# Kernel tuning notes

Measured on AMD Instinct MI355X. Metric: run time of the kernel, lower is better.

## Reference

```python
import jax, jax.numpy as jnp
import numpy as np

BLOCKS, LAYERS, KS = 4, 2, 2
DILATIONS = [2 ** i for _ in range(BLOCKS) for i in range(LAYERS)]  # [1,2]*4
B, C_IN, N, T = 16, 2, 2048, 12
RC, DC, SC, EC, OUT = 32, 32, 256, 512, 12
L = BLOCKS * LAYERS
BN_EPS = 1e-5


def setup_inputs() -> dict:
    key = jax.random.key(0)
    ks = jax.random.split(key, 24)
    # raw inputs
    x = jax.random.normal(ks[0], (B, C_IN, N, T), dtype=jnp.float32)
    # two fixed supports: row-normalized random adjacency (dense, as in GraphWaveNet transition matrices)
    A_raw = jax.random.uniform(ks[1], (2, N, N), dtype=jnp.float32)
    A = A_raw / jnp.sum(A_raw, axis=2, keepdims=True)
    nodevec1 = jax.random.normal(ks[2], (N, 10), dtype=jnp.float32)
    nodevec2 = jax.random.normal(ks[3], (10, N), dtype=jnp.float32)
    s = 0.1  # weight scale to keep activations in a sane range
    filter_w = jax.random.normal(ks[4], (L, DC, RC, KS), dtype=jnp.float32) * s
    filter_b = jax.random.normal(ks[5], (L, DC), dtype=jnp.float32) * s
    gate_w = jax.random.normal(ks[6], (L, DC, RC, KS), dtype=jnp.float32) * s
    gate_b = jax.random.normal(ks[7], (L, DC), dtype=jnp.float32) * s
    skip_w = jax.random.normal(ks[8], (L, SC, DC), dtype=jnp.float32) * s
    skip_b = jax.random.normal(ks[9], (L, SC), dtype=jnp.float32) * s
    gcn_w = jax.random.normal(ks[10], (L, RC, 7 * DC), dtype=jnp.float32) * s
    gcn_b = jax.random.normal(ks[11], (L, RC), dtype=jnp.float32) * s
    bn_gamma = 1.0 + 0.1 * jax.random.normal(ks[12], (L, RC), dtype=jnp.float32)
    bn_beta = 0.1 * jax.random.normal(ks[13], (L, RC), dtype=jnp.float32)
    bn_mean = 0.1 * jax.random.normal(ks[14], (L, RC), dtype=jnp.float32)
    bn_var = 1.0 + jax.random.uniform(ks[15], (L, RC), dtype=jnp.float32)
    start_w = jax.random.normal(ks[16], (RC, C_IN), dtype=jnp.float32) * s
    start_b = jax.random.normal(ks[17], (RC,), dtype=jnp.float32) * s
    end1_w = jax.random.normal(ks[18], (EC, SC), dtype=jnp.float32) * s
    end1_b = jax.random.normal(ks[19], (EC,), dtype=jnp.float32) * s
    end2_w = jax.random.normal(ks[20], (OUT, EC), dtype=jnp.float32) * s
    end2_b = jax.random.normal(ks[21], (OUT,), dtype=jnp.float32) * s
    return dict(x=x, A=A, nodevec1=nodevec1, nodevec2=nodevec2,
                filter_w=filter_w, filter_b=filter_b, gate_w=gate_w, gate_b=gate_b,
                skip_w=skip_w, skip_b=skip_b, gcn_w=gcn_w, gcn_b=gcn_b,
                bn_gamma=bn_gamma, bn_beta=bn_beta, bn_mean=bn_mean, bn_var=bn_var,
                start_w=start_w, start_b=start_b, end1_w=end1_w, end1_b=end1_b,
                end2_w=end2_w, end2_b=end2_b)


def _conv1x1(x, w, b):
    # x: [b,c,n,t], w: [o,c] -> [b,o,n,t]
    return jnp.einsum('oc,bcnt->bont', w, x) + b[None, :, None, None]


def _dilated_conv2(x, w, b, d):
    # kernel (1,2) with time dilation d; out length T-d (valid conv)
    xa, xb = x[..., :-d], x[..., d:]
    y = jnp.einsum('oc,bcnt->bont', w[:, :, 0], xa) + jnp.einsum('oc,bcnt->bont', w[:, :, 1], xb)
    return y + b[None, :, None, None]


def _fwd(x, A, nodevec1, nodevec2, filter_w, filter_b, gate_w, gate_b,
         skip_w, skip_b, gcn_w, gcn_b, bn_gamma, bn_beta, bn_mean, bn_var,
         start_w, start_b, end1_w, end1_b, end2_w, end2_b):
    # pad 1 step at the start of time; T becomes 13 == receptive_field
    x = jnp.pad(x, ((0, 0), (0, 0), (0, 0), (1, 0)))
    x = x[:, :2]
    x = _conv1x1(x, start_w, start_b)  # [B,RC,N,13]
    # adaptive adjacency
    adp = jax.nn.softmax(jax.nn.relu(nodevec1 @ nodevec2), axis=1)
    supports = [A[0], A[1], adp]
    skip = None
    for i, d in enumerate(DILATIONS):
        residual = x
        filt = jnp.tanh(_dilated_conv2(residual, filter_w[i], filter_b[i], d))
        gate = jax.nn.sigmoid(_dilated_conv2(residual, gate_w[i], gate_b[i], d))
        x = filt * gate  # [B,DC,N,T-d]
        s = _conv1x1(x, skip_w[i], skip_b[i])  # [B,SC,N,T']
        skip = s if skip is None else s + skip[..., -s.shape[3]:]
        # GCN: order-2 diffusion over 3 supports, concat, 1x1 mix (dropout is identity in eval)
        outs = [x]
        for a in supports:
            x1 = jnp.einsum('bcvt,vw->bcwt', x, a)
            x2 = jnp.einsum('bcvt,vw->bcwt', x1, a)
            outs.extend([x1, x2])
        h = jnp.concatenate(outs, axis=1)  # [B,7*DC,N,T']
        x = _conv1x1(h, gcn_w[i], gcn_b[i])
        x = x + residual[..., -x.shape[3]:]
        # BatchNorm2d in eval mode (running stats)
        inv = bn_gamma[i] / jnp.sqrt(bn_var[i] + BN_EPS)
        x = (x - bn_mean[i][None, :, None, None]) * inv[None, :, None, None] + bn_beta[i][None, :, None, None]
    x = jax.nn.relu(skip)
    x = jax.nn.relu(_conv1x1(x, end1_w, end1_b))
    x = _conv1x1(x, end2_w, end2_b)  # [B,OUT,N,1]
    return x


def reference(x, A, nodevec1, nodevec2, filter_w, filter_b, gate_w, gate_b,
              skip_w, skip_b, gcn_w, gcn_b, bn_gamma, bn_beta, bn_mean, bn_var,
              start_w, start_b, end1_w, end1_b, end2_w, end2_b):
    return _fwd(x, A, nodevec1, nodevec2, filter_w, filter_b, gate_w, gate_b,
                skip_w, skip_b, gcn_w, gcn_b, bn_gamma, bn_beta, bn_mean, bn_var,
                start_w, start_b, end1_w, end1_b, end2_w, end2_b)
```

## Files before the change

### kernel.cpp

```cpp
#include <hip/hip_runtime.h>
#include <math.h>


#define NNODE 2048
#define NLAYER 8
#define SSTR ((size_t)NNODE * NNODE)

typedef unsigned short u16;
typedef unsigned int u32;
typedef __attribute__((ext_vector_type(8))) short bf16x8;
typedef __attribute__((ext_vector_type(4))) float f32x4;

__device__ __forceinline__ u16 f2bf(float f) {
    unsigned u = __builtin_bit_cast(unsigned, f);
    u += 0x7fffu + ((u >> 16) & 1u);
    return (u16)(u >> 16);
}
__device__ __forceinline__ float bf2f(u16 h) {
    unsigned u = ((unsigned)h) << 16;
    return __builtin_bit_cast(float, u);
}
__device__ __forceinline__ float bflo(u32 p) { return __builtin_bit_cast(float, p << 16); }
__device__ __forceinline__ float bfhi(u32 p) { return __builtin_bit_cast(float, p & 0xffff0000u); }
__device__ __forceinline__ u32 pack2(float a, float b) {
    return (u32)f2bf(a) | ((u32)f2bf(b) << 16);
}

__device__ __forceinline__ void gld16(const void* g, void* l) {
    __builtin_amdgcn_global_load_lds(
        (const __attribute__((address_space(1))) unsigned int*)g,
        (__attribute__((address_space(3))) unsigned int*)l, 16, 0, 0);
}

__global__ __launch_bounds__(256) void k_adp_mm(const float* __restrict__ nv1,
                                                const float* __restrict__ nv2,
                                                float* __restrict__ P) {
    int v = blockIdx.y;
    int w = blockIdx.x * 256 + threadIdx.x;
    float acc = 0.f;
#pragma unroll
    for (int k = 0; k < 10; ++k) acc += nv1[v * 10 + k] * nv2[k * NNODE + w];
    P[(size_t)v * NNODE + w] = acc;
}

__global__ __launch_bounds__(256) void k_softmax(float* __restrict__ P) {
    int v = blockIdx.x, tid = threadIdx.x;
    float* row = P + (size_t)v * NNODE;
    float m = 0.f;
    for (int w = tid; w < NNODE; w += 256) m = fmaxf(m, fmaxf(row[w], 0.f));
#pragma unroll
    for (int off = 32; off > 0; off >>= 1) m = fmaxf(m, __shfl_down(m, off));
    __shared__ float redm[4];
    __shared__ float reds[4];
    int wave = tid >> 6, lane = tid & 63;
    if (lane == 0) redm[wave] = m;
    __syncthreads();
    m = fmaxf(fmaxf(redm[0], redm[1]), fmaxf(redm[2], redm[3]));
    float s = 0.f;
    for (int w = tid; w < NNODE; w += 256) s += expf(fmaxf(row[w], 0.f) - m);
#pragma unroll
    for (int off = 32; off > 0; off >>= 1) s += __shfl_down(s, off);
    if (lane == 0) reds[wave] = s;
    __syncthreads();
    s = reds[0] + reds[1] + reds[2] + reds[3];
    float inv = 1.f / s;
    for (int w = tid; w < NNODE; w += 256) row[w] = expf(fmaxf(row[w], 0.f) - m) * inv;
}

__global__ __launch_bounds__(256) void k_transp(const float* __restrict__ A,
                                                const float* __restrict__ adp,
                                                u16* __restrict__ ST,
                                                u16* __restrict__ Sbf) {
    __shared__ float tile[32][33];
    int s = blockIdx.z;
    const float* src = (s < 2) ? (A + (size_t)s * SSTR) : adp;
    int v0 = blockIdx.y * 32, w0 = blockIdx.x * 32;
    int tx = threadIdx.x & 31, ty = threadIdx.x >> 5;
    u16* dst2 = Sbf + (size_t)s * SSTR;
#pragma unroll
    for (int p = 0; p < 4; ++p) {
        float v = src[(size_t)(v0 + ty + p * 8) * NNODE + w0 + tx];
        tile[ty + p * 8][tx] = v;
        dst2[(size_t)(v0 + ty + p * 8) * NNODE + w0 + tx] = f2bf(v);
    }
    __syncthreads();
    u16* dst = ST + (size_t)(2 * s) * SSTR;
#pragma unroll
    for (int p = 0; p < 4; ++p)
        dst[(size_t)(w0 + ty + p * 8) * NNODE + v0 + tx] = f2bf(tile[tx][ty + p * 8]);
}

__global__ __launch_bounds__(256) void k_gemm_mfma(
    const u16* __restrict__ A, int lda, size_t asstr,
    const u16* __restrict__ BT, size_t bsstr,
    u16* __restrict__ C, int ldc, size_t csstr, int sbase) {
    __shared__ u16 Asl[128 * 32];
    __shared__ u16 Bsl[128 * 32];
    const int tid = threadIdx.x;
    const int wave = tid >> 6, lane = tid & 63;
    const int sidx = sbase + blockIdx.z;
    const u16* Ab = A + sidx * asstr + (size_t)blockIdx.y * 128 * lda;
    const u16* Bb = BT + sidx * bsstr + (size_t)blockIdx.x * 128 * NNODE;
    const int tr = tid >> 2;
    const int tc = (tid & 3) * 8;
    char* AslB = (char*)Asl + wave * 1024;
    char* BslB = (char*)Bsl + wave * 1024;
    const int wm = (wave & 1) * 64, wn = (wave >> 1) * 64;
    const int fr = lane & 15;
    const int fk = (lane >> 4) * 8;
    f32x4 acc[4][4];
#pragma unroll
    for (int i = 0; i < 4; ++i)
#pragma unroll
        for (int j = 0; j < 4; ++j) acc[i][j] = (f32x4){0.f, 0.f, 0.f, 0.f};

    for (int k0 = 0; k0 < 2048; k0 += 32) {
        gld16(Ab + (size_t)tr * lda + k0 + tc, AslB);
        gld16(Ab + (size_t)(tr + 64) * lda + k0 + tc, AslB + 4096);
        gld16(Bb + (size_t)tr * NNODE + k0 + tc, BslB);
        gld16(Bb + (size_t)(tr + 64) * NNODE + k0 + tc, BslB + 4096);
        __syncthreads();
        bf16x8 af[4], bf[4];
#pragma unroll
        for (int i = 0; i < 4; ++i)
            af[i] = *(const bf16x8*)&Asl[(wm + i * 16 + fr) * 32 + fk];
#pragma unroll
        for (int j = 0; j < 4; ++j)
            bf[j] = *(const bf16x8*)&Bsl[(wn + j * 16 + fr) * 32 + fk];
#pragma unroll
        for (int i = 0; i < 4; ++i)
#pragma unroll
            for (int j = 0; j < 4; ++j)
                acc[i][j] = __builtin_amdgcn_mfma_f32_16x16x32_bf16(af[i], bf[j], acc[i][j], 0, 0, 0);
        __syncthreads();
    }
    u16* Cb = C + sidx * csstr + (size_t)(blockIdx.y * 128 + wm) * ldc + blockIdx.x * 128 + wn;
    const int orow = (lane >> 4) * 4;
#pragma unroll
    for (int i = 0; i < 4; ++i)
#pragma unroll
        for (int j = 0; j < 4; ++j)
#pragma unroll
            for (int r = 0; r < 4; ++r)
                Cb[(size_t)(i * 16 + orow + r) * ldc + j * 16 + fr] = f2bf(acc[i][j][r]);
}

__global__ __launch_bounds__(512, 2) void k_gemmZ(const u16* __restrict__ Xg,
                                                  const u16* __restrict__ ST,
                                                  u16* __restrict__ Z, int pass) {
    __shared__ __align__(16) char ldsb[131072];
    const int tid = threadIdx.x;
    const int wave = tid >> 6, lane = tid & 63;
    const int m0 = blockIdx.y * 256;
    const int slice = pass * 3 + (blockIdx.x >> 3);
    const int n0 = (blockIdx.x & 7) * 256;
    const u16* AbG = Xg + (size_t)m0 * 2048;
    const u16* BbG = ST + (size_t)slice * SSTR + (size_t)n0 * 2048;

    const int xorc = ((tid & 7) ^ ((tid >> 3) & 7)) << 3;
    const size_t aRow = (size_t)(tid >> 3) * 2048 + xorc;
    const int bRowLoc = ((tid >> 8) << 6) + (((tid >> 6) & 3) << 3) + ((tid >> 3) & 7);
    const size_t bRow = (size_t)bRowLoc * 2048 + xorc;
    const int aw = wave << 10;
    const int bw = ((wave >> 2) << 13) + ((wave & 3) << 10);

    const int fr = lane & 15;
    const int cl4 = lane >> 4;
    const int ch0 = (cl4 ^ (fr & 7)) << 4;
    const int ch1 = ch0 ^ 64;
    const int aRd = ((wave & 1) << 14) + fr * 128;
    const int bRd = ((wave >> 1) << 13) + fr * 128;
    const int wm = (wave & 1) << 7;
    const int wn = (wave >> 1) << 6;

    char* A0 = ldsb;
    char* A1 = ldsb + 32768;
    char* B0 = ldsb + 65536;
    char* B1 = ldsb + 98304;

    auto STA = [&](char* Abase, int k0, int q) {
        const size_t g = (size_t)(q << 6) * 2048 + aRow + k0;
        gld16(AbG + g, Abase + (q << 13) + aw);
        gld16(AbG + g + (size_t)128 * 2048, Abase + 16384 + (q << 13) + aw);
    };
    auto STB = [&](char* Bbase, int k0, int q) {
        const size_t g = (size_t)(q << 5) * 2048 + bRow + k0;
        gld16(BbG + g, Bbase + (q << 12) + bw);
        gld16(BbG + g + (size_t)128 * 2048, Bbase + 16384 + (q << 12) + bw);
    };

    f32x4 acc[8][4];
#pragma unroll
    for (int i = 0; i < 8; ++i)
#pragma unroll
        for (int j = 0; j < 4; ++j) acc[i][j] = (f32x4){0.f, 0.f, 0.f, 0.f};

    STA(A0, 0, 0); STA(A0, 0, 1); STB(B0, 0, 0); STB(B0, 0, 1);
    STA(A1, 64, 0); STB(B1, 64, 0); STB(B1, 64, 1);
    asm volatile("s_waitcnt vmcnt(6)" ::: "memory");
    asm volatile("s_barrier" ::: "memory");

    char *Ac = A0, *Ao = A1, *Bc = B0, *Bo = B1;
    bf16x8 af[4][2], bfl[2][2], bfh[2][2];

    for (int T = 0; T < 32; ++T) {
#pragma unroll
        for (int i = 0; i < 4; ++i) {
            af[i][0] = *(const bf16x8*)(Ac + aRd + (i << 11) + ch0);
            af[i][1] = *(const bf16x8*)(Ac + aRd + (i << 11) + ch1);
        }
#pragma unroll
        for (int j = 0; j < 2; ++j) {
            bfl[j][0] = *(const bf16x8*)(Bc + bRd + (j << 11) + ch0);
            bfl[j][1] = *(const bf16x8*)(Bc + bRd + (j << 11) + ch1);
        }
        if (T < 31) STA(Ao, (T + 1) * 64, 1);
        asm volatile("s_barrier" ::: "memory");
        asm volatile("s_waitcnt lgkmcnt(0)" ::: "memory");
        __builtin_amdgcn_sched_barrier(0);
        __builtin_amdgcn_s_setprio(1);
#pragma unroll
        for (int i = 0; i < 4; ++i)
#pragma unroll
            for (int j = 0; j < 2; ++j) {
                acc[i][j] = __builtin_amdgcn_mfma_f32_16x16x32_bf16(af[i][0], bfl[j][0], acc[i][j], 0, 0, 0);
                acc[i][j] = __builtin_amdgcn_mfma_f32_16x16x32_bf16(af[i][1], bfl[j][1], acc[i][j], 0, 0, 0);
            }
        __builtin_amdgcn_s_setprio(0);
        asm volatile("s_barrier" ::: "memory");
#pragma unroll
        for (int j = 0; j < 2; ++j) {
            bfh[j][0] = *(const bf16x8*)(Bc + bRd + 4096 + (j << 11) + ch0);
            bfh[j][1] = *(const bf16x8*)(Bc + bRd + 4096 + (j << 11) + ch1);
        }
        if (T < 30) STA(Ac, (T + 2) * 64, 0);
        asm volatile("s_barrier" ::: "memory");
        asm volatile("s_waitcnt lgkmcnt(0)" ::: "memory");
        __builtin_amdgcn_sched_barrier(0);
        __builtin_amdgcn_s_setprio(1);
#pragma unroll
        for (int i = 0; i < 4; ++i)
#pragma unroll
            for (int j = 0; j < 2; ++j) {
                acc[i][2 + j] = __builtin_amdgcn_mfma_f32_16x16x32_bf16(af[i][0], bfh[j][0], acc[i][2 + j], 0, 0, 0);
                acc[i][2 + j] = __builtin_amdgcn_mfma_f32_16x16x32_bf16(af[i][1], bfh[j][1], acc[i][2 + j], 0, 0, 0);
            }
        __builtin_amdgcn_s_setprio(0);
        asm volatile("s_barrier" ::: "memory");
#pragma unroll
        for (int i = 0; i < 4; ++i) {
            af[i][0] = *(const bf16x8*)(Ac + aRd + 8192 + (i << 11) + ch0);
            af[i][1] = *(const bf16x8*)(Ac + aRd + 8192 + (i << 11) + ch1);
        }
        if (T < 30) STB(Bc, (T + 2) * 64, 0);
        asm volatile("s_barrier" ::: "memory");
        asm volatile("s_waitcnt lgkmcnt(0)" ::: "memory");
        __builtin_amdgcn_sched_barrier(0);
        __builtin_amdgcn_s_setprio(1);
#pragma unroll
        for (int i = 0; i < 4; ++i)
#pragma unroll
            for (int j = 0; j < 2; ++j) {
                acc[4 + i][2 + j] = __builtin_amdgcn_mfma_f32_16x16x32_bf16(af[i][0], bfh[j][0], acc[4 + i][2 + j], 0, 0, 0);
                acc[4 + i][2 + j] = __builtin_amdgcn_mfma_f32_16x16x32_bf16(af[i][1], bfh[j][1], acc[4 + i][2 + j], 0, 0, 0);
            }
        __builtin_amdgcn_s_setprio(0);
        asm volatile("s_barrier" ::: "memory");
        if (T < 30) STB(Bc, (T + 2) * 64, 1);
        asm volatile("s_barrier" ::: "memory");
        __builtin_amdgcn_sched_barrier(0);
        __builtin_amdgcn_s_setprio(1);
#pragma unroll
        for (int i = 0; i < 4; ++i)
#pragma unroll
            for (int j = 0; j < 2; ++j) {
                acc[4 + i][j] = __builtin_amdgcn_mfma_f32_16x16x32_bf16(af[i][0], bfl[j][0], acc[4 + i][j], 0, 0, 0);
                acc[4 + i][j] = __builtin_amdgcn_mfma_f32_16x16x32_bf16(af[i][1], bfl[j][1], acc[4 + i][j], 0, 0, 0);
            }
        __builtin_amdgcn_s_setprio(0);
        if (T < 30) {
            asm volatile("s_waitcnt vmcnt(6)" ::: "memory");
        } else if (T == 30) {
            asm volatile("s_waitcnt vmcnt(0)" ::: "memory");
        }
        asm volatile("s_barrier" ::: "memory");
        char* t;
        t = Ac; Ac = Ao; Ao = t;
        t = Bc; Bc = Bo; Bo = t;
    }

    const int col0 = (blockIdx.x >> 3) * 2048 + (blockIdx.x & 7) * 256;
    u16* Cb = Z + (size_t)(m0 + wm) * 6144 + col0 + wn;
    const int orow = cl4 * 4;
#pragma unroll
    for (int i = 0; i < 8; ++i)
#pragma unroll
        for (int j = 0; j < 4; ++j)
#pragma unroll
            for (int r = 0; r < 4; ++r)
                Cb[(size_t)(i * 16 + orow + r) * 6144 + j * 16 + fr] = f2bf(acc[i][j][r]);
}

__global__ __launch_bounds__(256) void k_start(const float* __restrict__ xin,
                                               const float* __restrict__ sw,
                                               const float* __restrict__ sb,
                                               u16* __restrict__ out, int b0) {
    int n = blockIdx.x * 256 + threadIdx.x;
    int t = blockIdx.y;
    int bl = blockIdx.z;
    int b = b0 + bl;
    float x0 = 0.f, x1 = 0.f;
    if (t > 0) {
        x0 = xin[((size_t)(b * 2 + 0) * NNODE + n) * 12 + (t - 1)];
        x1 = xin[((size_t)(b * 2 + 1) * NNODE + n) * 12 + (t - 1)];
    }
#pragma unroll
    for (int co = 0; co < 32; ++co) {
        float v = sw[co * 2 + 0] * x0 + sw[co * 2 + 1] * x1 + sb[co];
        out[((size_t)(bl * 32 + co) * 13 + t) * NNODE + n] = f2bf(v);
    }
}

__global__ __launch_bounds__(256) void k_gate(const u16* __restrict__ cur,
                                              u16* __restrict__ xg,
                                              u16* __restrict__ nxt,
                                              int T, int Tn, int d,
                                              const float* __restrict__ fw,
                                              const float* __restrict__ fb,
                                              const float* __restrict__ gw,
                                              const float* __restrict__ gb,
                                              const float* __restrict__ gcwl,
                                              const float* __restrict__ gcbl,
                                              int donxt) {
    __shared__ float4 wp[1024];
    __shared__ float w0[32][33];
    int tid = threadIdx.x;
#pragma unroll
    for (int u = 0; u < 4; ++u) {
        int idx = tid + u * 256;
        int ci = idx >> 5, co = idx & 31;
        wp[idx] = make_float4(fw[co * 64 + ci * 2], fw[co * 64 + ci * 2 + 1],
                              gw[co * 64 + ci * 2], gw[co * 64 + ci * 2 + 1]);
        w0[ci][co] = gcwl[co * 224 + ci];
    }
    __syncthreads();
    int n = blockIdx.x * 512 + tid * 2;
    int t = blockIdx.y;
    int bl = blockIdx.z;
    float f0[32], f1[32], g0[32], g1[32];
#pragma unroll
    for (int co = 0; co < 32; ++co) { f0[co] = 0.f; f1[co] = 0.f; g0[co] = 0.f; g1[co] = 0.f; }
    for (int ci = 0; ci < 32; ++ci) {
        size_t ba = ((size_t)(bl * 32 + ci) * T + t) * NNODE + n;
        size_t bb = ((size_t)(bl * 32 + ci) * T + t + d) * NNODE + n;
        u32 ua = *(const u32*)&cur[ba];
        u32 ub = *(const u32*)&cur[bb];
        float xa0 = bflo(ua), xa1 = bfhi(ua);
        float xb0 = bflo(ub), xb1 = bfhi(ub);
#pragma unroll
        for (int co = 0; co < 32; ++co) {
            float4 w = wp[ci * 32 + co];
            f0[co] += w.x * xa0 + w.y * xb0;
            f1[co] += w.x * xa1 + w.y * xb1;
            g0[co] += w.z * xa0 + w.w * xb0;
            g1[co] += w.z * xa1 + w.w * xb1;
        }
    }
#pragma unroll
    for (int co = 0; co < 32; ++co) {
        float fbv = fb[co], gbv = gb[co];
        float a0 = tanhf(f0[co] + fbv) * (1.f / (1.f + expf(-(g0[co] + gbv))));
        float a1 = tanhf(f1[co] + fbv) * (1.f / (1.f + expf(-(g1[co] + gbv))));
        f0[co] = a0; f1[co] = a1;
        size_t o = ((size_t)(bl * 32 + co) * Tn + t) * NNODE + n;
        *(u32*)&xg[o] = pack2(a0, a1);
    }
    if (donxt) {
#pragma unroll
        for (int cop = 0; cop < 32; ++cop) {
            float s0 = gcbl[cop], s1 = s0;
#pragma unroll
            for (int ci = 0; ci < 32; ++ci) {
                float wv = w0[ci][cop];
                s0 += wv * f0[ci];
                s1 += wv * f1[ci];
            }
            size_t o = ((size_t)(bl * 32 + cop) * Tn + t) * NNODE + n;
            *(u32*)&nxt[o] = pack2(s0, s1);
        }
    }
}

__global__ __launch_bounds__(256) void k_skip(const u16* __restrict__ xg,
                                              float* __restrict__ skip, int Tn,
                                              const float* __restrict__ sw,
                                              const float* __restrict__ sb, int b0, int init) {
    __shared__ float wl[256];
    int tid = threadIdx.x;
    int sc0 = blockIdx.y * 8;
    wl[tid] = sw[sc0 * 32 + tid];
    __syncthreads();
    int n = blockIdx.x * 512 + tid * 2;
    int bl = blockIdx.z;
    float a0[8], a1[8];
#pragma unroll
    for (int j = 0; j < 8; ++j) { a0[j] = 0.f; a1[j] = 0.f; }
    for (int ci = 0; ci < 32; ci += 2) {
        u32 p0 = *(const u32*)&xg[((size_t)(bl * 32 + ci + 0) * Tn + (Tn - 1)) * NNODE + n];
        u32 p1 = *(const u32*)&xg[((size_t)(bl * 32 + ci + 1) * Tn + (Tn - 1)) * NNODE + n];
        float v00 = bflo(p0), v01 = bfhi(p0);
        float v10 = bflo(p1), v11 = bfhi(p1);
#pragma unroll
        for (int j = 0; j < 8; ++j) {
            float wA = wl[j * 32 + ci], wB = wl[j * 32 + ci + 1];
            a0[j] += wA * v00 + wB * v10;
            a1[j] += wA * v01 + wB * v11;
        }
    }
    int b = b0 + bl;
#pragma unroll
    for (int j = 0; j < 8; ++j) {
        size_t o = ((size_t)(b * 256) + sc0 + j) * NNODE + n;
        float bsv = sb[sc0 + j];
        if (init) {
            *(float2*)&skip[o] = make_float2(a0[j] + bsv, a1[j] + bsv);
        } else {
            float2 old = *(const float2*)&skip[o];
            *(float2*)&skip[o] = make_float2(old.x + a0[j] + bsv, old.y + a1[j] + bsv);
        }
    }
}

__global__ __launch_bounds__(256) void k_accum(const u16* __restrict__ Z,
                                               int cbase,
                                               const float* __restrict__ gcnw,
                                               u16* __restrict__ outp,
                                               const u16* __restrict__ resid,
                                               int Tn, int d, int finalf,
                                               const float* __restrict__ bng,
                                               const float* __restrict__ bnb,
                                               const float* __restrict__ bnm,
                                               const float* __restrict__ bnv) {
    __shared__ float wl[3][32][32];
    int tid = threadIdx.x;
    for (int u = tid; u < 3072; u += 256) {
        int g = u >> 10, ci = (u >> 5) & 31, co = u & 31;
        wl[g][ci][co] = gcnw[co * 224 + cbase + g * 32 + ci];
    }
    __syncthreads();
    int n = blockIdx.x * 512 + tid * 2;
    int t = blockIdx.y, bl = blockIdx.z;
    float a0[32], a1[32];
#pragma unroll
    for (int co = 0; co < 32; ++co) { a0[co] = 0.f; a1[co] = 0.f; }
    for (int ci = 0; ci < 32; ++ci) {
        size_t m = (size_t)(bl * 32 + ci) * Tn + t;
#pragma unroll
        for (int g = 0; g < 3; ++g) {
            u32 zz = *(const u32*)&Z[m * 6144 + g * 2048 + n];
            float v0 = bflo(zz), v1 = bfhi(zz);
#pragma unroll
            for (int cq = 0; cq < 8; ++cq) {
                float4 w = *(const float4*)&wl[g][ci][cq * 4];
                a0[cq * 4 + 0] += w.x * v0; a1[cq * 4 + 0] += w.x * v1;
                a0[cq * 4 + 1] += w.y * v0; a1[cq * 4 + 1] += w.y * v1;
                a0[cq * 4 + 2] += w.z * v0; a1[cq * 4 + 2] += w.z * v1;
                a0[cq * 4 + 3] += w.w * v0; a1[cq * 4 + 3] += w.w * v1;
            }
        }
    }
#pragma unroll
    for (int co = 0; co < 32; ++co) {
        size_t o = ((size_t)(bl * 32 + co) * Tn + t) * NNODE + n;
        u32 oo = *(const u32*)&outp[o];
        float v0 = bflo(oo) + a0[co];
        float v1 = bfhi(oo) + a1[co];
        if (finalf) {
            size_t ro = ((size_t)(bl * 32 + co) * (Tn + d) + t + d) * NNODE + n;
            u32 rr = *(const u32*)&resid[ro];
            v0 += bflo(rr); v1 += bfhi(rr);
            float inv = bng[co] * rsqrtf(bnv[co] + 1e-5f);
            float mu = bnm[co], be = bnb[co];
            v0 = (v0 - mu) * inv + be;
            v1 = (v1 - mu) * inv + be;
        }
        *(u32*)&outp[o] = pack2(v0, v1);
    }
}

__global__ __launch_bounds__(256) void k_skipT(const float* __restrict__ skip,
                                               u16* __restrict__ skipT) {
    __shared__ float tile[32][33];
    int b = blockIdx.z;
    int n0 = blockIdx.x * 32, c0 = blockIdx.y * 32;
    int tx = threadIdx.x & 31, ty = threadIdx.x >> 5;
#pragma unroll
    for (int p = 0; p < 4; ++p)
        tile[ty + p * 8][tx] = skip[((size_t)b * 256 + c0 + ty + p * 8) * NNODE + n0 + tx];
    __syncthreads();
#pragma unroll
    for (int p = 0; p < 4; ++p)
        skipT[((size_t)b * NNODE + n0 + ty + p * 8) * 256 + c0 + tx] =
            f2bf(fmaxf(tile[tx][ty + p * 8], 0.f));
}

__global__ __launch_bounds__(256) void k_cast(const float* __restrict__ src,
                                              u16* __restrict__ dst) {
    int i = blockIdx.x * 256 + threadIdx.x;
    dst[i] = f2bf(src[i]);
}

__global__ __launch_bounds__(256) void k_end1m(const u16* __restrict__ E1,
                                               const u16* __restrict__ skT,
                                               const float* __restrict__ bias,
                                               u16* __restrict__ h) {
    __shared__ u16 Asl[128 * 32];
    __shared__ u16 Bsl[128 * 32];
    const int tid = threadIdx.x;
    const int wave = tid >> 6, lane = tid & 63;
    const int b = blockIdx.z;
    const int m0 = blockIdx.y * 128;
    const int n0 = blockIdx.x * 128;
    const int tr = tid >> 2;
    const int tc = (tid & 3) * 8;
    char* AslB = (char*)Asl + wave * 1024;
    char* BslB = (char*)Bsl + wave * 1024;
    const int wm = (wave & 1) * 64, wn = (wave >> 1) * 64;
    const int fr = lane & 15;
    const int fk = (lane >> 4) * 8;
    const u16* Ab = E1 + (size_t)m0 * 256;
    const u16* Bb = skT + ((size_t)b * NNODE + n0) * 256;
    f32x4 acc[4][4];
#pragma unroll
    for (int i = 0; i < 4; ++i)
#pragma unroll
        for (int j = 0; j < 4; ++j) acc[i][j] = (f32x4){0.f, 0.f, 0.f, 0.f};
    for (int k0 = 0; k0 < 256; k0 += 32) {
        gld16(Ab + (size_t)tr * 256 + k0 + tc, AslB);
        gld16(Ab + (size_t)(tr + 64) * 256 + k0 + tc, AslB + 4096);
        gld16(Bb + (size_t)tr * 256 + k0 + tc, BslB);
        gld16(Bb + (size_t)(tr + 64) * 256 + k0 + tc, BslB + 4096);
        __syncthreads();
        bf16x8 af[4], bf[4];
#pragma unroll
        for (int i = 0; i < 4; ++i)
            af[i] = *(const bf16x8*)&Asl[(wm + i * 16 + fr) * 32 + fk];
#pragma unroll
        for (int j = 0; j < 4; ++j)
            bf[j] = *(const bf16x8*)&Bsl[(wn + j * 16 + fr) * 32 + fk];
#pragma unroll
        for (int i = 0; i < 4; ++i)
#pragma unroll
            for (int j = 0; j < 4; ++j)
                acc[i][j] = __builtin_amdgcn_mfma_f32_16x16x32_bf16(af[i], bf[j], acc[i][j], 0, 0, 0);
        __syncthreads();
    }
    const int orow = (lane >> 4) * 4;
#pragma unroll
    for (int i = 0; i < 4; ++i)
#pragma unroll
        for (int r = 0; r < 4; ++r) {
            int m = m0 + wm + i * 16 + orow + r;
            float bs = bias[m];
            size_t ob = ((size_t)b * 512 + m) * NNODE + n0 + wn;
#pragma unroll
            for (int j = 0; j < 4; ++j)
                h[ob + j * 16 + fr] = f2bf(fmaxf(acc[i][j][r] + bs, 0.f));
        }
}

__global__ __launch_bounds__(256) void k_end2(const u16* __restrict__ h,
                                              const float* __restrict__ w,
                                              const float* __restrict__ bias,
                                              float* __restrict__ out) {
    __shared__ float wl[12][512];
    int tid = threadIdx.x;
    for (int u = tid; u < 6144; u += 256) wl[u >> 9][u & 511] = w[u];
    __syncthreads();
    int n = blockIdx.x * 256 + tid;
    int b = blockIdx.y;
    float acc[12];
#pragma unroll
    for (int o = 0; o < 12; ++o) acc[o] = 0.f;
#pragma unroll 4
    for (int e = 0; e < 512; ++e) {
        float v = bf2f(h[((size_t)(b * 512) + e) * NNODE + n]);
#pragma unroll
        for (int o = 0; o < 12; ++o) acc[o] += wl[o][e] * v;
    }
#pragma unroll
    for (int o = 0; o < 12; ++o)
        out[((size_t)(b * 12) + o) * NNODE + n] = acc[o] + bias[o];
}

extern "C" void kernel_launch(void* const* d_in, const int* in_sizes, int n_in,
                              void* d_out, int out_size, void* d_ws, size_t ws_size,
                              hipStream_t stream) {
    const float* x_in = (const float*)d_in[0];
    const float* A    = (const float*)d_in[1];
    const float* nv1  = (const float*)d_in[2];
    const float* nv2  = (const float*)d_in[3];
    const float* fw   = (const float*)d_in[4];
    const float* fb   = (const float*)d_in[5];
    const float* gw   = (const float*)d_in[6];
    const float* gb   = (const float*)d_in[7];
    const float* skw  = (const float*)d_in[8];
    const float* skb  = (const float*)d_in[9];
    const float* gcw  = (const float*)d_in[10];
    const float* gcb  = (const float*)d_in[11];
    const float* bng  = (const float*)d_in[12];
    const float* bnb  = (const float*)d_in[13];
    const float* bnm  = (const float*)d_in[14];
    const float* bnv  = (const float*)d_in[15];
    const float* stw  = (const float*)d_in[16];
    const float* stb  = (const float*)d_in[17];
    const float* e1w  = (const float*)d_in[18];
    const float* e1b  = (const float*)d_in[19];
    const float* e2w  = (const float*)d_in[20];
    const float* e2b  = (const float*)d_in[21];
    (void)in_sizes; (void)n_in; (void)out_size;

    const int BL = (ws_size >= 239075328UL) ? 16 : 8;
    const int nch = 16 / BL;
    const size_t bufsz = (size_t)BL * 1703936UL;

    char* base = (char*)d_ws;
    u16*   ST   = (u16*)base;
    float* skip = (float*)(base + 50331648UL);
    u16*   bufA = (u16*)(base + 83886080UL);
    u16*   bufB = (u16*)(base + 83886080UL + bufsz);
    u16*   xg   = (u16*)(base + 83886080UL + 2 * bufsz);
    u16*   Z    = (u16*)(base + 83886080UL + 2 * bufsz + (size_t)BL * 1572864UL);
    float* adp  = (float*)Z;
    u16*   Sbf  = (u16*)bufA;
    u16*   h     = (u16*)(base + 83886080UL);
    u16*   skipT = (u16*)(base + 83886080UL + 33554432UL);
    u16*   E1bf  = (u16*)ST;

    k_adp_mm<<<dim3(8, 2048), 256, 0, stream>>>(nv1, nv2, adp);
    k_softmax<<<2048, 256, 0, stream>>>(adp);
    k_transp<<<dim3(64, 64, 3), 256, 0, stream>>>(A, adp, ST, Sbf);
    k_gemm_mfma<<<dim3(16, 16, 3), 256, 0, stream>>>(
        ST, NNODE, 2 * SSTR, Sbf, SSTR, ST + SSTR, NNODE, 2 * SSTR, 0);

    static const int DIL[NLAYER] = {1, 2, 1, 2, 1, 2, 1, 2};
    for (int ch = 0; ch < nch; ++ch) {
        int b0 = ch * BL;
        k_start<<<dim3(8, 13, BL), 256, 0, stream>>>(x_in, stw, stb, bufA, b0);
        u16* cur = bufA;
        u16* nxt = bufB;
        int T = 13;
        for (int i = 0; i < NLAYER; ++i) {
            int d = DIL[i], Tn = T - d;
            int last = (i == NLAYER - 1);
            k_gate<<<dim3(4, Tn, BL), 256, 0, stream>>>(cur, xg, nxt, T, Tn, d,
                fw + i * 2048, fb + i * 32, gw + i * 2048, gb + i * 32,
                gcw + i * 32 * 224, gcb + i * 32, last ? 0 : 1);
            k_skip<<<dim3(4, 32, BL), 256, 0, stream>>>(xg, skip, Tn,
                skw + i * 256 * 32, skb + i * 256, b0, (i == 0) ? 1 : 0);
            if (last) break;
            int MB = BL * Tn / 8;
            const float* gcwi = gcw + i * 32 * 224;
            for (int p = 0; p < 2; ++p) {
                k_gemmZ<<<dim3(24, MB), 512, 0, stream>>>(xg, ST, Z, p);
                k_accum<<<dim3(4, Tn, BL), 256, 0, stream>>>(
                    Z, 32 + 96 * p, gcwi, nxt, cur, Tn, d, p,
                    bng + i * 32, bnb + i * 32, bnm + i * 32, bnv + i * 32);
            }
            u16* tmp = cur; cur = nxt; nxt = tmp;
            T = Tn;
        }
    }
    k_cast<<<512, 256, 0, stream>>>(e1w, E1bf);
    k_skipT<<<dim3(64, 8, 16), 256, 0, stream>>>(skip, skipT);
    k_end1m<<<dim3(16, 4, 16), 256, 0, stream>>>(E1bf, skipT, e1b, h);
    k_end2<<<dim3(8, 16), 256, 0, stream>>>(h, e2w, e2b, (float*)d_out);
}
```

Measured before the change: 3.134 ms.

## Add 128x128 GEMM tile for small-T layers and trim barriers in main GEMM

Adds a k_gemmZ128 kernel with 128x128 tiles and 256 threads. It is used for layers whose output time length is 6 or 3, where the large-tile kernel launches too few blocks to fill the GPU. It also removes several s_barriers from the pipelined 256-tile GEMM and merges two LDS stores into one phase to cut synchronisation stalls. The barrier removal risks an LDS read/write hazard if the buffer reuse ordering was relied on, and the new kernel has a simpler, non-overlapped load loop.

```diff
diff --git a/kernel.cpp b/kernel.cpp
--- a/kernel.cpp
+++ b/kernel.cpp
@@ -227,13 +227,11 @@
                 acc[i][j] = __builtin_amdgcn_mfma_f32_16x16x32_bf16(af[i][1], bfl[j][1], acc[i][j], 0, 0, 0);
             }
         __builtin_amdgcn_s_setprio(0);
-        asm volatile("s_barrier" ::: "memory");
 #pragma unroll
         for (int j = 0; j < 2; ++j) {
             bfh[j][0] = *(const bf16x8*)(Bc + bRd + 4096 + (j << 11) + ch0);
             bfh[j][1] = *(const bf16x8*)(Bc + bRd + 4096 + (j << 11) + ch1);
         }
-        if (T < 30) STA(Ac, (T + 2) * 64, 0);
         asm volatile("s_barrier" ::: "memory");
         asm volatile("s_waitcnt lgkmcnt(0)" ::: "memory");
         __builtin_amdgcn_sched_barrier(0);
@@ -246,13 +244,12 @@
                 acc[i][2 + j] = __builtin_amdgcn_mfma_f32_16x16x32_bf16(af[i][1], bfh[j][1], acc[i][2 + j], 0, 0, 0);
             }
         __builtin_amdgcn_s_setprio(0);
-        asm volatile("s_barrier" ::: "memory");
 #pragma unroll
         for (int i = 0; i < 4; ++i) {
             af[i][0] = *(const bf16x8*)(Ac + aRd + 8192 + (i << 11) + ch0);
             af[i][1] = *(const bf16x8*)(Ac + aRd + 8192 + (i << 11) + ch1);
         }
-        if (T < 30) STB(Bc, (T + 2) * 64, 0);
+        if (T < 30) { STA(Ac, (T + 2) * 64, 0); STB(Bc, (T + 2) * 64, 0); }
         asm volatile("s_barrier" ::: "memory");
         asm volatile("s_waitcnt lgkmcnt(0)" ::: "memory");
         __builtin_amdgcn_sched_barrier(0);
@@ -265,7 +262,6 @@
                 acc[4 + i][2 + j] = __builtin_amdgcn_mfma_f32_16x16x32_bf16(af[i][1], bfh[j][1], acc[4 + i][2 + j], 0, 0, 0);
             }
         __builtin_amdgcn_s_setprio(0);
-        asm volatile("s_barrier" ::: "memory");
         if (T < 30) STB(Bc, (T + 2) * 64, 1);
         asm volatile("s_barrier" ::: "memory");
         __builtin_amdgcn_sched_barrier(0);
@@ -294,6 +290,71 @@
     const int orow = cl4 * 4;
 #pragma unroll
     for (int i = 0; i < 8; ++i)
+#pragma unroll
+        for (int j = 0; j < 4; ++j)
+#pragma unroll
+            for (int r = 0; r < 4; ++r)
+                Cb[(size_t)(i * 16 + orow + r) * 6144 + j * 16 + fr] = f2bf(acc[i][j][r]);
+}
+
+__global__ __launch_bounds__(256) void k_gemmZ128(const u16* __restrict__ Xg,
+                                                  const u16* __restrict__ ST,
+                                                  u16* __restrict__ Z, int pass) {
+    __shared__ u16 Asl[2][128 * 32];
+    __shared__ u16 Bsl[2][128 * 32];
+    const int tid = threadIdx.x;
+    const int wave = tid >> 6, lane = tid & 63;
+    const int m0 = blockIdx.y * 128;
+    const int slice = pass * 3 + (blockIdx.x >> 4);
+    const int nIn = (blockIdx.x & 15) * 128;
+    const u16* Ab = Xg + (size_t)m0 * 2048;
+    const u16* Bb = ST + (size_t)slice * SSTR + (size_t)nIn * NNODE;
+    const int tr = tid >> 2;
+    const int tc = (tid & 3) * 8;
+    char* AslB0 = (char*)Asl[0] + wave * 1024;
+    char* AslB1 = (char*)Asl[1] + wave * 1024;
+    char* BslB0 = (char*)Bsl[0] + wave * 1024;
+    char* BslB1 = (char*)Bsl[1] + wave * 1024;
+    const int wm = (wave & 1) * 64, wn = (wave >> 1) * 64;
+    const int fr = lane & 15;
+    const int fk = (lane >> 4) * 8;
+    f32x4 acc[4][4];
+#pragma unroll
+    for (int i = 0; i < 4; ++i)
+#pragma unroll
+        for (int j = 0; j < 4; ++j) acc[i][j] = (f32x4){0.f, 0.f, 0.f, 0.f};
+
+    for (int k0 = 0; k0 < 2048; k0 += 64) {
+        gld16(Ab + (size_t)tr * 2048 + k0 + tc, AslB0);
+        gld16(Ab + (size_t)(tr + 64) * 2048 + k0 + tc, AslB0 + 4096);
+        gld16(Ab + (size_t)tr * 2048 + k0 + 32 + tc, AslB1);
+        gld16(Ab + (size_t)(tr + 64) * 2048 + k0 + 32 + tc, AslB1 + 4096);
+        gld16(Bb + (size_t)tr * NNODE + k0 + tc, BslB0);
+        gld16(Bb + (size_t)(tr + 64) * NNODE + k0 + tc, BslB0 + 4096);
+        gld16(Bb + (size_t)tr * NNODE + k0 + 32 + tc, BslB1);
+        gld16(Bb + (size_t)(tr + 64) * NNODE + k0 + 32 + tc, BslB1 + 4096);
+        __syncthreads();
+#pragma unroll
+        for (int h = 0; h < 2; ++h) {
+            bf16x8 af[4], bf[4];
+#pragma unroll
+            for (int i = 0; i < 4; ++i)
+                af[i] = *(const bf16x8*)&Asl[h][(wm + i * 16 + fr) * 32 + fk];
+#pragma unroll
+            for (int j = 0; j < 4; ++j)
+                bf[j] = *(const bf16x8*)&Bsl[h][(wn + j * 16 + fr) * 32 + fk];
+#pragma unroll
+            for (int i = 0; i < 4; ++i)
+#pragma unroll
+                for (int j = 0; j < 4; ++j)
+                    acc[i][j] = __builtin_amdgcn_mfma_f32_16x16x32_bf16(af[i], bf[j], acc[i][j], 0, 0, 0);
+        }
+        __syncthreads();
+    }
+    u16* Cb = Z + (size_t)(m0 + wm) * 6144 + blockIdx.x * 128 + wn;
+    const int orow = (lane >> 4) * 4;
+#pragma unroll
+    for (int i = 0; i < 4; ++i)
 #pragma unroll
         for (int j = 0; j < 4; ++j)
 #pragma unroll
@@ -659,10 +720,13 @@
             k_skip<<<dim3(4, 32, BL), 256, 0, stream>>>(xg, skip, Tn,
                 skw + i * 256 * 32, skb + i * 256, b0, (i == 0) ? 1 : 0);
             if (last) break;
-            int MB = BL * Tn / 8;
             const float* gcwi = gcw + i * 32 * 224;
             for (int p = 0; p < 2; ++p) {
-                k_gemmZ<<<dim3(24, MB), 512, 0, stream>>>(xg, ST, Z, p);
+                if (Tn == 6 || Tn == 3) {
+                    k_gemmZ128<<<dim3(48, BL * Tn / 4), 256, 0, stream>>>(xg, ST, Z, p);
+                } else {
+                    k_gemmZ<<<dim3(24, BL * 32 * Tn / 256), 512, 0, stream>>>(xg, ST, Z, p);
+                }
                 k_accum<<<dim3(4, Tn, BL), 256, 0, stream>>>(
                     Z, 32 + 96 * p, gcwi, nxt, cur, Tn, d, p,
                     bng + i * 32, bnb + i * 32, bnm + i * 32, bnv + i * 32);
```

New measurement: 3.023 ms. -3.6%, faster.
